# Performance work log

Hardware: AMD Instinct MI355X
Metric: run time of the kernel (lower is better)

## Reference

```python
import jax, jax.numpy as jnp
import numpy as np

B, T, BIN, D, S, L = 128, 512, 24, 256, 128, 2
MAX_LEN = 512.0   # config.max_length, used as attention score scale
EPS = 1e-6
P = 3.0           # GeM pooling power


def _sinusoid(t, dim, min_ts=1.0, max_ts=10000.0):
    # half sin / half cos geometric timescales (min_timescale..max_timescale)
    num = dim // 2
    inv = min_ts * jnp.exp(jnp.arange(num, dtype=jnp.float32) * (-np.log(max_ts / min_ts) / max(num - 1, 1)))
    ang = jnp.arange(t, dtype=jnp.float32)[:, None] * inv[None, :]        # [T, dim/2]
    return jnp.concatenate([jnp.sin(ang), jnp.cos(ang)], axis=-1)          # [T, dim]


def _rope(x):
    # rotate-half RoPE over last dim, positions along axis -2
    t, d = x.shape[-2], x.shape[-1]
    inv = 1.0 / (10000.0 ** (jnp.arange(0, d, 2, dtype=jnp.float32) / d))  # [d/2]
    ang = jnp.arange(t, dtype=jnp.float32)[:, None] * inv[None, :]         # [T, d/2]
    sin = jnp.concatenate([jnp.sin(ang), jnp.sin(ang)], axis=-1)
    cos = jnp.concatenate([jnp.cos(ang), jnp.cos(ang)], axis=-1)
    x1, x2 = jnp.split(x, 2, axis=-1)
    return x * cos + jnp.concatenate([-x2, x1], axis=-1) * sin


def setup_inputs() -> dict:
    key = jax.random.key(0)
    ks = jax.random.split(key, 12)
    std_in = 1.0 / np.sqrt(BIN)
    std_d = 1.0 / np.sqrt(D)
    return {
        "x": jax.random.uniform(ks[0], (B, T, BIN), dtype=jnp.float32),
        "pe_scale": jnp.ones((), jnp.float32),                                  # learnable PE scale
        "W_in": jax.random.normal(ks[1], (BIN, D), jnp.float32) * std_in,        # encoder_start
        "b_in": jnp.zeros((D,), jnp.float32),
        "norm_scale": jnp.ones((L,), jnp.float32),                               # ScaledNorm scalar per layer
        "W1": jax.random.normal(ks[2], (L, D, 2 * D + S), jnp.float32) * std_d,  # GAU in-proj
        "b1": jnp.zeros((L, 2 * D + S), jnp.float32),
        "gamma": jnp.ones((L, 2, S), jnp.float32),                               # q/k offset-scale
        "beta": jnp.zeros((L, 2, S), jnp.float32),
        "W2": jax.random.normal(ks[3], (L, D, D), jnp.float32) * std_d,          # GAU out-proj
        "b2": jnp.zeros((L, D), jnp.float32),
        "We": jax.random.normal(ks[4], (D, D), jnp.float32) * std_d,             # metric embedding
        "be": jnp.zeros((D,), jnp.float32),
    }


def reference(x, pe_scale, W_in, b_in, norm_scale, W1, b1, gamma, beta, W2, b2, We, be):
    # scaled sinusoidal positional embedding (additive)
    h = x + pe_scale * _sinusoid(x.shape[1], x.shape[2])
    # encoder start + swish
    h = jax.nn.swish(h @ W_in + b_in)                                   # [B,T,D]
    for i in range(L):  # GAU stack (attention-free gated attention units)
        shortcut = h
        hn = h * jax.lax.rsqrt(jnp.mean(h * h, axis=-1, keepdims=True) + EPS) * norm_scale[i]
        uv = jax.nn.swish(hn @ W1[i] + b1[i])                           # [B,T,2D+S]
        u, v, base = uv[..., :D], uv[..., D:2 * D], uv[..., 2 * D:]
        q = _rope(base * gamma[i, 0] + beta[i, 0])                      # [B,T,S]
        k = _rope(base * gamma[i, 1] + beta[i, 1])
        scores = jnp.einsum('bnd,bmd->bnm', q, k) / MAX_LEN             # [B,T,T]
        attn = jnp.square(jax.nn.relu(scores))                          # SqrReLU
        out = u * jnp.einsum('bnm,bme->bne', attn, v)                   # gated attention output
        h = shortcut + out @ W2[i] + b2[i]
    unpooled = h
    # generalized-mean pooling over sequence (p=3, clamp for stability)
    pooled = jnp.mean(jnp.clip(h, EPS, None) ** P, axis=1) ** (1.0 / P)  # [B,D]
    # metric embedding: linear + L2 normalize
    emb = pooled @ We + be
    emb = emb / jnp.linalg.norm(emb, axis=-1, keepdims=True)
    return emb, unpooled
```

## Files before the change

kernel.cpp:

```cpp
#include <hip/hip_runtime.h>
#include <hip/hip_bf16.h>

#define B_ 128
#define T_ 512
#define BIN_ 24
#define D_ 256
#define S_ 128
#define L_ 2
#define BT_ (B_*T_)

typedef __hip_bfloat16 bf16;
typedef __hip_bfloat162 bf162;
typedef __attribute__((ext_vector_type(8))) short bf16x8;
typedef __attribute__((ext_vector_type(4))) short s16x4;
typedef __attribute__((ext_vector_type(4))) float f32x4;

__device__ __forceinline__ float b2f(bf16 x){ return __bfloat162float(x); }
__device__ __forceinline__ bf16 f2b(float x){ return __float2bfloat16(x); }
__device__ __forceinline__ float swish(float v){
  float e = __builtin_amdgcn_exp2f(-1.442695040888963f * v);
  return v * __builtin_amdgcn_rcpf(1.f + e);
}
__device__ __forceinline__ void gld16(const bf16* g, bf16* l){
  __builtin_amdgcn_global_load_lds(
      (const __attribute__((address_space(1))) void*)g,
      (__attribute__((address_space(3))) void*)l, 16, 0, 0);
}

__global__ void tables_kernel(const float* pe_scale_ptr, float* pe_tab, float* rs, float* rc) {
  int t = blockIdx.x;
  int j = threadIdx.x;
  float ps = pe_scale_ptr[0];
  const float LOG1E4 = 9.210340371976184f;
  if (j < 64) {
    float inv = expf(-LOG1E4 * (float)j / 64.f);
    float ang = (float)t * inv;
    rs[t*64 + j] = sinf(ang);
    rc[t*64 + j] = cosf(ang);
  }
  if (j < BIN_) {
    int jj = (j < 12) ? j : (j - 12);
    float inv = expf(-LOG1E4 * (float)jj / 11.f);
    float ang = (float)t * inv;
    pe_tab[t*BIN_ + j] = ps * ((j < 12) ? sinf(ang) : cosf(ang));
  }
}

__global__ __launch_bounds__(256) void prep_kernel(const float* W1, const float* W2,
                                                   bf16* W1t, bf16* W2t) {
  int idx = blockIdx.x*256 + threadIdx.x;
  if (idx < 2*256*640) {
    int l = idx / (256*640); int rem = idx % (256*640);
    int k = rem / 640; int n = rem % 640;
    W1t[(size_t)l*640*256 + n*256 + k] = f2b(W1[idx]);
  }
  if (idx < 2*256*256) {
    int l = idx >> 16; int rem = idx & 65535;
    int k = rem >> 8; int n = rem & 255;
    W2t[(size_t)l*65536 + n*256 + k] = f2b(W2[idx]);
  }
}

__global__ __launch_bounds__(256) void init_kernel(float* rms1, float* pooled_raw) {
  int i = blockIdx.x*256 + threadIdx.x;
  if (i < BT_) rms1[i] = 0.f;
  if (i < B_*D_) pooled_raw[i] = 0.f;
}

__global__ __launch_bounds__(256) void embed_kernel(const float* x, const float* pe_tab,
                const float* W_in, const float* b_in, float* h, float* rms0, bf16* hb) {
  __shared__ float xr[8][BIN_];
  __shared__ float wsum[4][8];
  int tid = threadIdx.x;
  int row0 = blockIdx.x * 8;
  if (tid < 8*BIN_) {
    int r = tid / BIN_, k = tid % BIN_;
    int row = row0 + r;
    int t = row & (T_-1);
    xr[r][k] = x[(size_t)row*BIN_ + k] + pe_tab[t*BIN_ + k];
  }
  __syncthreads();
  int d = tid;
  float bi = b_in[d];
  float acc[8];
  #pragma unroll
  for (int r=0;r<8;r++) acc[r]=bi;
  #pragma unroll
  for (int k=0;k<BIN_;k++){
    float w = W_in[k*D_ + d];
    #pragma unroll
    for (int r=0;r<8;r++) acc[r] += xr[r][k]*w;
  }
  float sq[8];
  #pragma unroll
  for (int r=0;r<8;r++){
    float v = swish(acc[r]);
    h[(size_t)(row0+r)*D_ + d] = v;
    hb[(size_t)(row0+r)*D_ + d] = f2b(v);
    sq[r] = v*v;
  }
  #pragma unroll
  for (int off=1; off<64; off<<=1)
    #pragma unroll
    for (int r=0;r<8;r++) sq[r] += __shfl_xor(sq[r], off);
  if ((tid&63)==0)
    #pragma unroll
    for (int r=0;r<8;r++) wsum[tid>>6][r] = sq[r];
  __syncthreads();
  if (tid < 8) rms0[row0+tid] = wsum[0][tid]+wsum[1][tid]+wsum[2][tid]+wsum[3][tid];
}

__global__ __launch_bounds__(256) void gemm1_mfma(const bf16* A, const bf16* Bt,
      const float* bias, const float* rmsraw, const float* norm_scale, int l,
      bf16* u, bf16* Vtg, bf16* basebuf) {
  __shared__ char smem[34816];
  bf16* As  = (bf16*)smem;
  bf16* Bs  = (bf16*)(smem + 16384);
  bf16* Ovl = (bf16*)smem;

  int tid = threadIdx.x;
  int w = tid>>6, lane = tid&63, r = lane&15, g = lane>>4;
  int wr = w>>1, wc = w&1;
  int dd = blockIdx.x; int xcd = dd&7, slot = dd>>3;
  int panel = xcd*64 + slot/5; int bx = slot%5;
  int row0 = panel*128, col0 = bx*128;

  int trl = 8*w + (lane>>3);
  int tcg = ((lane&7) ^ ((lane>>3)&7)) * 8;

  f32x4 acc[4][4];
  #pragma unroll
  for (int i=0;i<4;i++)
    #pragma unroll
    for (int j=0;j<4;j++) acc[i][j] = (f32x4){0.f,0.f,0.f,0.f};

  for (int k0=0; k0<D_; k0+=64) {
    #pragma unroll
    for (int i=0;i<4;i++){
      int tr = 32*i + trl;
      gld16(A  + (size_t)(row0+tr)*D_ + k0 + tcg, As + (32*i + 8*w)*64);
      gld16(Bt + (size_t)(col0+tr)*D_ + k0 + tcg, Bs + (32*i + 8*w)*64);
    }
    __syncthreads();
    #pragma unroll
    for (int kk=0; kk<2; kk++){
      bf16x8 a[4], b[4];
      #pragma unroll
      for (int i=0;i<4;i++){
        int ch = ((kk*4 + g) ^ (r&7)) * 8;
        a[i] = *(const bf16x8*)(As + (64*wr+16*i+r)*64 + ch);
        b[i] = *(const bf16x8*)(Bs + (64*wc+16*i+r)*64 + ch);
      }
      #pragma unroll
      for (int i=0;i<4;i++)
        #pragma unroll
        for (int j=0;j<4;j++)
          acc[i][j] = __builtin_amdgcn_mfma_f32_16x16x32_bf16(a[i], b[j], acc[i][j], 0,0,0);
    }
    __syncthreads();
  }

  float ns = norm_scale[l];
  #pragma unroll
  for (int i=0;i<4;i++){
    size_t grow0 = row0 + 64*wr + 16*i + 4*g;
    float4 rv = *(const float4*)(rmsraw + grow0);
    float sc[4];
    sc[0] = rsqrtf(rv.x*(1.f/D_) + 1e-6f) * ns;
    sc[1] = rsqrtf(rv.y*(1.f/D_) + 1e-6f) * ns;
    sc[2] = rsqrtf(rv.z*(1.f/D_) + 1e-6f) * ns;
    sc[3] = rsqrtf(rv.w*(1.f/D_) + 1e-6f) * ns;
    #pragma unroll
    for (int j=0;j<4;j++){
      int gcol = col0 + 64*wc + 16*j + r;
      float bv = bias[gcol];
      if (bx == 2 || bx == 3) {
        #pragma unroll
        for (int reg=0; reg<4; reg++){
          float v = swish(acc[i][j][reg]*sc[reg] + bv);
          Ovl[(64*wc+16*j+r)*136 + (64*wr+16*i+4*g+reg)] = f2b(v);
        }
      } else {
        #pragma unroll
        for (int reg=0; reg<4; reg++){
          float v = swish(acc[i][j][reg]*sc[reg] + bv);
          Ovl[(64*wr+16*i+4*g+reg)*136 + (64*wc+16*j+r)] = f2b(v);
        }
      }
    }
  }

  __syncthreads();
  if (bx == 2 || bx == 3) {
    size_t bb = row0 >> 9;
    int mg = row0 & 511;
    #pragma unroll
    for (int c=0;c<8;c++){
      int chunk = c*256 + tid;
      int e = chunk >> 4, mloc = (chunk & 15)*8;
      *(bf16x8*)(Vtg + bb*131072 + (size_t)(col0-256+e)*T_ + mg + mloc) =
        *(const bf16x8*)(Ovl + e*136 + mloc);
    }
  } else {
    #pragma unroll
    for (int c=0;c<8;c++){
      int chunk = c*256 + tid;
      int lr = chunk >> 4, lc = (chunk & 15)*8;
      bf16x8 v = *(const bf16x8*)(Ovl + lr*136 + lc);
      if (bx < 2)
        *(bf16x8*)(u + (size_t)(row0+lr)*D_ + col0 + lc) = v;
      else
        *(bf16x8*)(basebuf + (size_t)(row0+lr)*S_ + lc) = v;
    }
  }
}

__global__ __launch_bounds__(256) void qk_kernel(const bf16* basebuf, const float* gamma, const float* beta,
      int l, const float* rs, const float* rc, bf16* q, bf16* k) {
  int tid = threadIdx.x;
  int j = tid & 127;
  size_t row = (size_t)blockIdx.x*2 + (tid>>7);
  int t = (int)(row & (T_-1));
  int j2 = j ^ 64;
  float v0 = b2f(basebuf[row*S_ + j]);
  float v1 = b2f(basebuf[row*S_ + j2]);
  int jm = j & 63;
  float sn = rs[t*64 + jm], cs = rc[t*64 + jm];
  float sgn = (j < 64) ? -1.f : 1.f;
  const float* g  = gamma + l*2*S_;
  const float* bt = beta  + l*2*S_;
  float xq = v0*g[j]      + bt[j];
  float pq = v1*g[j2]     + bt[j2];
  q[row*S_ + j] = f2b(xq*cs + sgn*pq*sn);
  float xk = v0*g[S_+j]   + bt[S_+j];
  float pk = v1*g[S_+j2]  + bt[S_+j2];
  k[row*S_ + j] = f2b(xk*cs + sgn*pk*sn);
}

__global__ __launch_bounds__(512, 4) void attn_gemm2_fused(const bf16* q, const bf16* k,
      const bf16* Vtg, const bf16* u, const bf16* W2t, const float* bias,
      float* h, int mode, float* rms1, float* pooled_raw, float* outb, bf16* hb) {
  __shared__ char smem[67584];
  bf16* Ks = (bf16*)smem;
  bf16* Vt = (bf16*)(smem + 16384);
  bf16* Ps = (bf16*)(smem + 49152);
  bf16* Os = (bf16*)smem;

  int tid = threadIdx.x;
  int w = tid >> 6, l = tid & 63;
  int r = l & 15, g = l >> 4;
  int xcd = blockIdx.x & 7, j0 = blockIdx.x >> 3;
  int b  = xcd*16 + (j0 >> 2);
  int nt = j0 & 3;
  size_t rowbase = (size_t)b * T_;
  int n0 = nt * 128;

  bf16x8 qf[4];
  const bf16* qrow = q + (rowbase + n0 + 16*w + r) * S_ + g*8;
  #pragma unroll
  for (int kk=0; kk<4; kk++) qf[kk] = *(const bf16x8*)(qrow + kk*32);

  f32x4 oacc[16];
  #pragma unroll
  for (int i=0;i<16;i++) oacc[i] = (f32x4){0.f,0.f,0.f,0.f};

  for (int m0 = 0; m0 < T_; m0 += 64) {
    #pragma unroll
    for (int i=0;i<2;i++){
      int chunk = i*512 + w*64 + l;
      int row = chunk >> 4, c = chunk & 15;
      gld16(k + (rowbase + m0 + row)*S_ + ((c ^ (row&7)) << 3),
            Ks + (i*512 + w*64)*8);
    }
    #pragma unroll
    for (int i=0;i<4;i++){
      int chunk = i*512 + w*64 + l;
      int e = chunk >> 3, c = chunk & 7;
      gld16(Vtg + (size_t)b*131072 + (size_t)e*T_ + m0 + ((c ^ (e&7)) << 3),
            Vt + (i*512 + w*64)*8);
    }
    __syncthreads();

    #pragma unroll
    for (int nf=0; nf<4; nf++){
      f32x4 sacc = (f32x4){0.f,0.f,0.f,0.f};
      #pragma unroll
      for (int kk=0; kk<4; kk++){
        int ch = ((kk*4 + g) ^ (r&7)) * 8;
        bf16x8 kf = *(const bf16x8*)(Ks + (16*nf + r)*128 + ch);
        sacc = __builtin_amdgcn_mfma_f32_16x16x32_bf16(qf[kk], kf, sacc, 0,0,0);
      }
      #pragma unroll
      for (int reg=0; reg<4; reg++){
        float t = fmaxf(sacc[reg] * (1.f/512.f), 0.f);
        Ps[(16*w + 4*g + reg)*72 + 16*nf + r] = f2b(t*t);
      }
    }
    #pragma unroll
    for (int ks=0; ks<2; ks++){
      bf16x8 pa = *(const bf16x8*)(Ps + (16*w + r)*72 + ks*32 + g*8);
      #pragma unroll
      for (int nf2=0; nf2<16; nf2++){
        int e = 16*nf2 + r;
        bf16x8 vb = *(const bf16x8*)(Vt + e*64 + (((4*ks + g) ^ (e&7)) << 3));
        oacc[nf2] = __builtin_amdgcn_mfma_f32_16x16x32_bf16(pa, vb, oacc[nf2], 0,0,0);
      }
    }
    __syncthreads();
  }

  size_t growbase = rowbase + n0;
  #pragma unroll
  for (int nf2=0; nf2<16; nf2++){
    #pragma unroll
    for (int reg=0; reg<4; reg++){
      Os[(16*w + 4*g + reg)*264 + 16*nf2 + r] = f2b(oacc[nf2][reg]);
    }
  }
  __syncthreads();
  #pragma unroll
  for (int i=0;i<8;i++){
    int chunk = i*512 + tid;
    int row = chunk >> 5, c = chunk & 31;
    bf16x8 uvv = *(const bf16x8*)(u + (growbase + row)*D_ + c*8);
    bf16x8 ov  = *(const bf16x8*)(Os + row*264 + c*8);
    bf16x8 res;
    #pragma unroll
    for (int e=0;e<8;e++)
      ((bf16*)&res)[e] = f2b(b2f(((bf16*)&ov)[e]) * b2f(((bf16*)&uvv)[e]));
    *(bf16x8*)(Os + row*264 + c*8) = res;
  }
  __syncthreads();

  #pragma unroll
  for (int chf=0; chf<2; chf++){
    int col = 128*chf + 16*w + r;
    bf16x8 wfr[8];
    #pragma unroll
    for (int kc=0; kc<8; kc++)
      wfr[kc] = *(const bf16x8*)(W2t + (size_t)col*256 + kc*32 + g*8);
    f32x4 acc2[8];
    #pragma unroll
    for (int i=0;i<8;i++) acc2[i] = (f32x4){0.f,0.f,0.f,0.f};
    #pragma unroll
    for (int kc=0; kc<8; kc++){
      #pragma unroll
      for (int i=0;i<8;i++){
        bf16x8 a0 = *(const bf16x8*)(Os + (16*i + r)*264 + kc*32 + g*8);
        acc2[i] = __builtin_amdgcn_mfma_f32_16x16x32_bf16(a0, wfr[kc], acc2[i], 0,0,0);
      }
    }

    float bv = bias[col];
    if (mode == 0) {
      #pragma unroll
      for (int i=0;i<8;i++){
        #pragma unroll
        for (int reg=0; reg<4; reg++){
          size_t row = growbase + 16*i + 4*g + reg;
          float hv = h[row*D_ + col] + acc2[i][reg] + bv;
          h[row*D_ + col] = hv;
          hb[row*D_ + col] = f2b(hv);
          float ssum = hv*hv;
          ssum += __shfl_xor(ssum,1); ssum += __shfl_xor(ssum,2);
          ssum += __shfl_xor(ssum,4); ssum += __shfl_xor(ssum,8);
          if (r == 0) atomicAdd(rms1 + row, ssum);
        }
      }
    } else {
      float psum = 0.f;
      #pragma unroll
      for (int i=0;i<8;i++){
        #pragma unroll
        for (int reg=0; reg<4; reg++){
          size_t row = growbase + 16*i + 4*g + reg;
          float hv = h[row*D_ + col] + acc2[i][reg] + bv;
          outb[row*D_ + col] = hv;
          float cv = fmaxf(hv, 1e-6f);
          psum += cv*cv*cv;
        }
      }
      psum += __shfl_xor(psum,16); psum += __shfl_xor(psum,32);
      if (g == 0) atomicAdd(pooled_raw + b*D_ + col, psum);
    }
  }
}

__global__ __launch_bounds__(256) void emb_kernel(const float* pooled_raw, const float* We,
      const float* be, float* out) {
  __shared__ float pr[D_];
  __shared__ float red[256];
  int b = blockIdx.x, j = threadIdx.x;
  pr[j] = cbrtf(pooled_raw[b*D_+j] * (1.f/T_));
  __syncthreads();
  float acc = be[j];
  for (int kk=0;kk<D_;kk++) acc += pr[kk]*We[kk*D_+j];
  red[j] = acc*acc;
  __syncthreads();
  for (int off=128; off>0; off>>=1){
    if (j<off) red[j]+=red[j+off];
    __syncthreads();
  }
  out[b*D_+j] = acc * rsqrtf(red[0]);
}

extern "C" void kernel_launch(void* const* d_in, const int* in_sizes, int n_in,
                              void* d_out, int out_size, void* d_ws, size_t ws_size,
                              hipStream_t stream) {
  const float* x         = (const float*)d_in[0];
  const float* pe_scale  = (const float*)d_in[1];
  const float* W_in      = (const float*)d_in[2];
  const float* b_in      = (const float*)d_in[3];
  const float* norm_scale= (const float*)d_in[4];
  const float* W1        = (const float*)d_in[5];
  const float* b1        = (const float*)d_in[6];
  const float* gamma     = (const float*)d_in[7];
  const float* beta      = (const float*)d_in[8];
  const float* W2        = (const float*)d_in[9];
  const float* b2        = (const float*)d_in[10];
  const float* We        = (const float*)d_in[11];
  const float* be        = (const float*)d_in[12];

  char* ws = (char*)d_ws;
  float* h       = (float*)(ws);
  bf16*  hb      = (bf16*)(ws + 67108864);
  bf16*  u       = (bf16*)(ws + 100663296);
  bf16*  Vtg     = (bf16*)(ws + 134217728);
  bf16*  basebuf = (bf16*)(ws + 167772160);
  bf16*  q       = (bf16*)(ws + 184549376);
  bf16*  kbuf    = (bf16*)(ws + 201326592);
  float* pe_tab  = (float*)(ws + 218103808);
  float* rs_tab  = (float*)(ws + 218152960);
  float* rc_tab  = (float*)(ws + 218284032);
  float* pooled_raw = (float*)(ws + 218415104);
  float* rms0    = (float*)(ws + 218546176);
  float* rms1    = (float*)(ws + 218808320);
  bf16*  W1t     = (bf16*)(ws + 219070464);
  bf16*  W2t     = (bf16*)(ws + 219725824);

  tables_kernel<<<T_, 64, 0, stream>>>(pe_scale, pe_tab, rs_tab, rc_tab);
  prep_kernel<<<1280, 256, 0, stream>>>(W1, W2, W1t, W2t);
  init_kernel<<<BT_/256, 256, 0, stream>>>(rms1, pooled_raw);
  embed_kernel<<<BT_/8, 256, 0, stream>>>(x, pe_tab, W_in, b_in, h, rms0, hb);
  float* outb = (float*)d_out + B_*D_;
  for (int l=0; l<L_; l++) {
    gemm1_mfma<<<BT_/128*5, 256, 0, stream>>>(hb, W1t + (size_t)l*640*D_, b1 + l*640,
        l ? rms1 : rms0, norm_scale, l, u, Vtg, basebuf);
    qk_kernel<<<BT_/2, 256, 0, stream>>>(basebuf, gamma, beta, l, rs_tab, rc_tab, q, kbuf);
    attn_gemm2_fused<<<B_*4, 512, 0, stream>>>(q, kbuf, Vtg, u,
        W2t + (size_t)l*D_*D_, b2 + l*D_, h, l, rms1, pooled_raw, outb, hb);
  }
  emb_kernel<<<B_, 256, 0, stream>>>(pooled_raw, We, be, (float*)d_out);
}
```

Measured before the change: 341.5 us.

## Retile PV and W2 MFMA loops to share operand fragments across two tiles

The P·V stage changes from each wave owning 16 query rows across all 256 output columns to a 2x4 wave grid: each wave covers 32 rows and 128 columns. Each V fragment read from LDS now feeds two MFMAs, which cuts V LDS traffic. This needs an extra block barrier between the P writes and the P reads. In the out-projection, each Os A-fragment is loaded once per k-chunk and reused for both column halves, instead of being reloaded per half. The cost is more live accumulators and registers in that stage.

Result: no change. 341.1 us (-0.1%).

```diff
diff --git a/kernel.cpp b/kernel.cpp
--- a/kernel.cpp
+++ b/kernel.cpp
@@ -249,6 +249,7 @@
   int tid = threadIdx.x;
   int w = tid >> 6, l = tid & 63;
   int r = l & 15, g = l >> 4;
+  int rgp = w & 3, eh = w >> 2;
   int xcd = blockIdx.x & 7, j0 = blockIdx.x >> 3;
   int b  = xcd*16 + (j0 >> 2);
   int nt = j0 & 3;
@@ -296,14 +297,18 @@
         Ps[(16*w + 4*g + reg)*72 + 16*nf + r] = f2b(t*t);
       }
     }
+    __syncthreads();
+
     #pragma unroll
     for (int ks=0; ks<2; ks++){
-      bf16x8 pa = *(const bf16x8*)(Ps + (16*w + r)*72 + ks*32 + g*8);
-      #pragma unroll
-      for (int nf2=0; nf2<16; nf2++){
-        int e = 16*nf2 + r;
+      bf16x8 pa0 = *(const bf16x8*)(Ps + (32*rgp      + r)*72 + ks*32 + g*8);
+      bf16x8 pa1 = *(const bf16x8*)(Ps + (32*rgp + 16 + r)*72 + ks*32 + g*8);
+      #pragma unroll
+      for (int ef=0; ef<8; ef++){
+        int e = 16*(8*eh + ef) + r;
         bf16x8 vb = *(const bf16x8*)(Vt + e*64 + (((4*ks + g) ^ (e&7)) << 3));
-        oacc[nf2] = __builtin_amdgcn_mfma_f32_16x16x32_bf16(pa, vb, oacc[nf2], 0,0,0);
+        oacc[ef]   = __builtin_amdgcn_mfma_f32_16x16x32_bf16(pa0, vb, oacc[ef],   0,0,0);
+        oacc[8+ef] = __builtin_amdgcn_mfma_f32_16x16x32_bf16(pa1, vb, oacc[8+ef], 0,0,0);
       }
     }
     __syncthreads();
@@ -311,12 +316,12 @@
 
   size_t growbase = rowbase + n0;
   #pragma unroll
-  for (int nf2=0; nf2<16; nf2++){
-    #pragma unroll
-    for (int reg=0; reg<4; reg++){
-      Os[(16*w + 4*g + reg)*264 + 16*nf2 + r] = f2b(oacc[nf2][reg]);
-    }
-  }
+  for (int rr=0; rr<2; rr++)
+    #pragma unroll
+    for (int ef=0; ef<8; ef++)
+      #pragma unroll
+      for (int reg=0; reg<4; reg++)
+        Os[(32*rgp + 16*rr + 4*g + reg)*264 + 16*(8*eh+ef) + r] = f2b(oacc[rr*8+ef][reg]);
   __syncthreads();
   #pragma unroll
   for (int i=0;i<8;i++){
@@ -332,25 +337,29 @@
   }
   __syncthreads();
 
+  f32x4 acc2[2][8];
+  #pragma unroll
+  for (int c2=0;c2<2;c2++)
+    #pragma unroll
+    for (int i=0;i<8;i++) acc2[c2][i] = (f32x4){0.f,0.f,0.f,0.f};
+  #pragma unroll
+  for (int kc=0; kc<8; kc++){
+    bf16x8 a0[8];
+    #pragma unroll
+    for (int i=0;i<8;i++)
+      a0[i] = *(const bf16x8*)(Os + (16*i + r)*264 + kc*32 + g*8);
+    #pragma unroll
+    for (int chf=0; chf<2; chf++){
+      bf16x8 wfr = *(const bf16x8*)(W2t + (size_t)(128*chf + 16*w + r)*256 + kc*32 + g*8);
+      #pragma unroll
+      for (int i=0;i<8;i++)
+        acc2[chf][i] = __builtin_amdgcn_mfma_f32_16x16x32_bf16(a0[i], wfr, acc2[chf][i], 0,0,0);
+    }
+  }
+
   #pragma unroll
   for (int chf=0; chf<2; chf++){
     int col = 128*chf + 16*w + r;
-    bf16x8 wfr[8];
-    #pragma unroll
-    for (int kc=0; kc<8; kc++)
-      wfr[kc] = *(const bf16x8*)(W2t + (size_t)col*256 + kc*32 + g*8);
-    f32x4 acc2[8];
-    #pragma unroll
-    for (int i=0;i<8;i++) acc2[i] = (f32x4){0.f,0.f,0.f,0.f};
-    #pragma unroll
-    for (int kc=0; kc<8; kc++){
-      #pragma unroll
-      for (int i=0;i<8;i++){
-        bf16x8 a0 = *(const bf16x8*)(Os + (16*i + r)*264 + kc*32 + g*8);
-        acc2[i] = __builtin_amdgcn_mfma_f32_16x16x32_bf16(a0, wfr[kc], acc2[i], 0,0,0);
-      }
-    }
-
     float bv = bias[col];
     if (mode == 0) {
       #pragma unroll
@@ -358,7 +367,7 @@
         #pragma unroll
         for (int reg=0; reg<4; reg++){
           size_t row = growbase + 16*i + 4*g + reg;
-          float hv = h[row*D_ + col] + acc2[i][reg] + bv;
+          float hv = h[row*D_ + col] + acc2[chf][i][reg] + bv;
           h[row*D_ + col] = hv;
           hb[row*D_ + col] = f2b(hv);
           float ssum = hv*hv;
@@ -374,7 +383,7 @@
         #pragma unroll
         for (int reg=0; reg<4; reg++){
           size_t row = growbase + 16*i + 4*g + reg;
-          float hv = h[row*D_ + col] + acc2[i][reg] + bv;
+          float hv = h[row*D_ + col] + acc2[chf][i][reg] + bv;
           outb[row*D_ + col] = hv;
           float cv = fmaxf(hv, 1e-6f);
           psum += cv*cv*cv;
```
